# Kernel optimization log

Hardware: AMD Instinct MI355X
Metric: run time of the kernel (lower is better)

The kernel has to match this reference:

```python
import jax, jax.numpy as jnp
import numpy as np

N, E, D_IN, D_E, H, OUT, L = 16384, 131072, 128, 64, 256, 16, 4
EPS_MSG = 1e-7   # GENConv message epsilon
EPS_SM = 1e-16   # PyG softmax denominator epsilon


def _ln(x, g, b, eps=1e-5):
    mu = x.mean(-1, keepdims=True)
    var = x.var(-1, keepdims=True)
    return (x - mu) * jax.lax.rsqrt(var + eps) * g + b


def _genconv(x, src, dst, e, w1, b1, lng, lnb, w2, b2, t):
    # message: relu(x_j + edge_attr) + eps  -> [E, H]
    msg = jax.nn.relu(x[src] + e) + EPS_MSG
    # learnable-temperature segment softmax over incoming edges, per feature
    m = msg * t
    mx = jax.ops.segment_max(m, dst, num_segments=N)
    mx = jnp.where(jnp.isfinite(mx), mx, 0.0)  # empty segments -> 0
    ex = jnp.exp(m - mx[dst])
    den = jax.ops.segment_sum(ex, dst, num_segments=N)
    alpha = ex / (den[dst] + EPS_SM)
    agg = jax.ops.segment_sum(msg * alpha, dst, num_segments=N)  # [N, H]
    # root residual then 2-layer MLP: Linear -> LayerNorm -> ReLU -> Linear
    out = agg + x
    h = jax.nn.relu(_ln(out @ w1 + b1, lng, lnb))
    return h @ w2 + b2


def setup_inputs() -> dict:
    key = jax.random.key(0)
    ks = jax.random.split(key, 10)
    gl = lambda k, shape, fan: jax.random.normal(k, shape, jnp.float32) / np.sqrt(fan).astype(np.float32)
    return {
        "x": jax.random.normal(ks[0], (N, D_IN), jnp.float32),
        "edge_index": jax.random.randint(ks[1], (2, E), 0, N, dtype=jnp.int32),
        "edge_attr": jax.random.normal(ks[2], (E, D_E), jnp.float32),
        "enc_w": gl(ks[3], (D_IN, H), D_IN), "enc_b": jnp.zeros((H,), jnp.float32),
        "ee_w": gl(ks[4], (D_E, H), D_E), "ee_b": jnp.zeros((H,), jnp.float32),
        "w1": gl(ks[5], (L, H, 2 * H), H), "b1": jnp.zeros((L, 2 * H), jnp.float32),
        "lng": jnp.ones((L, 2 * H), jnp.float32), "lnb": jnp.zeros((L, 2 * H), jnp.float32),
        "w2": gl(ks[6], (L, 2 * H, H), 2 * H), "b2": jnp.zeros((L, H), jnp.float32),
        "t": jnp.ones((L,), jnp.float32),
        "ng": jnp.ones((L, H), jnp.float32), "nb": jnp.zeros((L, H), jnp.float32),
        "lin_w": gl(ks[7], (H, OUT), H), "lin_b": jnp.zeros((OUT,), jnp.float32),
    }


def reference(x, edge_index, edge_attr, enc_w, enc_b, ee_w, ee_b,
              w1, b1, lng, lnb, w2, b2, t, ng, nb, lin_w, lin_b):
    src, dst = edge_index[0], edge_index[1]
    h = x @ enc_w + enc_b                      # node encoder
    e = edge_attr @ ee_w + ee_b                # edge encoder
    # first layer: conv only (per source forward)
    h = _genconv(h, src, dst, e, w1[0], b1[0], lng[0], lnb[0], w2[0], b2[0], t[0])
    # remaining layers: res+ block = x + conv(relu(norm(x)))  (dropout off in eval)
    for i in range(1, L):
        z = jax.nn.relu(_ln(h, ng[i], nb[i]))
        h = h + _genconv(z, src, dst, e, w1[i], b1[i], lng[i], lnb[i], w2[i], b2[i], t[i])
    h = jax.nn.relu(_ln(h, ng[0], nb[0]))      # layers[0].act(layers[0].norm(x))
    return h @ lin_w + lin_b
```

## Files before the change

kernel.cpp:

```cpp
#include <hip/hip_runtime.h>
#include <stdint.h>
#include <math.h>


typedef __bf16 bf16x8 __attribute__((ext_vector_type(8)));
typedef __bf16 bf16x4 __attribute__((ext_vector_type(4)));
typedef float  f32x4  __attribute__((ext_vector_type(4)));

constexpr int NN   = 16384;
constexpr int NE   = 131072;
constexpr int DIN  = 128;
constexpr int DE   = 64;
constexpr int HD   = 256;
constexpr int HD2  = 512;

__device__ __forceinline__ void gl_lds16(const __bf16* g, __bf16* l) {
  __builtin_amdgcn_global_load_lds((const __attribute__((address_space(1))) void*)g,
                                   (__attribute__((address_space(3))) void*)l, 16, 0, 0);
}

__global__ __launch_bounds__(1024) void k_scan(const int* __restrict__ deg,
                                               int* __restrict__ row_start) {
  __shared__ int part[1024];
  const int t = threadIdx.x;
  const int base = t * 16;
  int loc[16];
  int s = 0;
  #pragma unroll
  for (int i = 0; i < 16; i++) { loc[i] = s; s += deg[base + i]; }
  part[t] = s;
  __syncthreads();
  for (int off = 1; off < 1024; off <<= 1) {
    int v = (t >= off) ? part[t - off] : 0;
    __syncthreads();
    part[t] += v;
    __syncthreads();
  }
  const int excl = (t == 0) ? 0 : part[t - 1];
  #pragma unroll
  for (int i = 0; i < 16; i++) row_start[base + i] = excl + loc[i];
}

__global__ void k_scatter(const int* __restrict__ src, const int* __restrict__ dst,
                          const int* __restrict__ row_start, int* __restrict__ cursor,
                          int2* __restrict__ csr_es) {
  int e = blockIdx.x * 256 + threadIdx.x;
  if (e >= NE) return;
  const int d = dst[e];
  const int p = atomicAdd(&cursor[d], 1);
  csr_es[row_start[d] + p] = make_int2(e, src[e]);
}

__global__ __launch_bounds__(256)
void k_sortw(const int* __restrict__ row_start, const int* __restrict__ deg,
             int2* __restrict__ csr_es, int* __restrict__ posmap) {
  const int wv   = threadIdx.x >> 6;
  const int lane = threadIdx.x & 63;
  const int node = blockIdx.x * 4 + wv;
  if (node >= NN) return;
  const int st = __builtin_amdgcn_readfirstlane(row_start[node]);
  const int dg = __builtin_amdgcn_readfirstlane(deg[node]);
  if (dg <= 1) {
    if (dg == 1 && lane == 0) posmap[csr_es[st].x] = st;
    return;
  }
  if (dg <= 64) {
    int2 pr = make_int2(0x7fffffff, 0);
    if (lane < dg) pr = csr_es[st + lane];
    int rank = 0;
    for (int j = 0; j < dg; j++) {
      const int ej = __builtin_amdgcn_readlane(pr.x, j);
      if (lane < dg && ej < pr.x) rank++;
    }
    if (lane < dg) {
      csr_es[st + rank] = pr;
      posmap[pr.x] = st + rank;
    }
  } else if (lane == 0) {
    for (int a = 1; a < dg; a++) {
      int2 k = csr_es[st + a];
      int b = a - 1;
      while (b >= 0 && csr_es[st + b].x > k.x) { csr_es[st + b + 1] = csr_es[st + b]; b--; }
      csr_es[st + b + 1] = k;
    }
    for (int a = 0; a < dg; a++) posmap[csr_es[st + a].x] = st + a;
  }
}

__global__ void k_prep(const float* __restrict__ enc_w, const float* __restrict__ ee_w,
                       const float* __restrict__ w1, const float* __restrict__ w2,
                       const int* __restrict__ dst, int* __restrict__ deg,
                       __bf16* __restrict__ enc_wT, __bf16* __restrict__ ee_wT,
                       __bf16* __restrict__ w1T, __bf16* __restrict__ w2T) {
  int i = blockIdx.x * 256 + threadIdx.x;
  const int S0 = DIN * HD, S1 = DE * HD, S2 = 4 * HD * HD2, S3 = 4 * HD2 * HD;
  if (i < S0) { int k = i / HD, n = i % HD; enc_wT[n * DIN + k] = (__bf16)enc_w[i]; return; }
  i -= S0;
  if (i < S1) { int k = i / HD, n = i % HD; ee_wT[n * DE + k] = (__bf16)ee_w[i]; return; }
  i -= S1;
  if (i < S2) {
    int l = i / (HD * HD2), r = i % (HD * HD2), k = r / HD2, n = r % HD2;
    w1T[(size_t)l * HD * HD2 + (size_t)n * HD + k] = (__bf16)w1[i]; return;
  }
  i -= S2;
  if (i < S3) {
    int l = i / (HD2 * HD), r = i % (HD2 * HD), k = r / HD, n = r % HD;
    w2T[(size_t)l * HD2 * HD + (size_t)n * HD2 + k] = (__bf16)w2[i]; return;
  }
  i -= S3;
  if (i < NE) { atomicAdd(&deg[dst[i]], 1); return; }
}

template <int RES, int OBF, int STATS, int ESCAT, int AF32>
__global__ __launch_bounds__(256, 3)
void k_gemm(const void* __restrict__ Ap, const __bf16* __restrict__ BT,
            const float* __restrict__ bias, const float* __restrict__ R,
            float* __restrict__ Cf, __bf16* __restrict__ Cb,
            const int* __restrict__ posmap, float2* __restrict__ pstats,
            int M, int Nn, int K) {
  __shared__ __attribute__((aligned(16))) char smem[32768];
  __bf16* lsA0 = (__bf16*)smem;
  __bf16* lsA1 = (__bf16*)(smem + 8192);
  __bf16* lsB0 = (__bf16*)(smem + 16384);
  __bf16* lsB1 = (__bf16*)(smem + 24576);
  float (*sm)[129] = (float(*)[129])smem;
  float* sbias     = (float*)(smem + 16512);
  float2 (*pst4)[32] = (float2(*)[32])(smem + 17024);
  const __bf16* Ab = (const __bf16*)Ap;
  const float*  Af = (const float*)Ap;
  const int tid  = threadIdx.x;
  const int lane = tid & 63;
  const int wave = tid >> 6;
  const int ntn  = Nn >> 7;
  const int bid  = (int)blockIdx.x;
  const int bn   = (bid >> 3) % ntn;
  const int bm   = (bid & 7) + ((bid >> 3) / ntn) * 8;
  const size_t row0 = (size_t)bm * 128, col0 = (size_t)bn * 128;
  const int wr = (wave >> 1) * 64, wc = (wave & 1) * 64;
  const int ks = lane >> 4, fr = lane & 15;

  f32x4 acc[4][4] = {};

  const int arow = tid >> 2;
  const int aksg = (tid & 3) ^ ((arow >> 1) & 3);

  auto stageB = [&](__bf16* lb, int k0) {
    gl_lds16(BT + (col0 + arow) * K + k0 + aksg * 8, &lb[tid * 8]);
    gl_lds16(BT + (col0 + arow + 64) * K + k0 + aksg * 8, &lb[(tid + 256) * 8]);
  };
  auto stageA = [&](__bf16* la, int k0) {
    gl_lds16(Ab + (row0 + arow) * K + k0 + aksg * 8, &la[tid * 8]);
    gl_lds16(Ab + (row0 + arow + 64) * K + k0 + aksg * 8, &la[(tid + 256) * 8]);
  };
  float4 p0, p1, q0, q1;
  auto loadAf = [&](int k0) {
    const float* a0p = &Af[(row0 + arow) * K + k0 + aksg * 8];
    const float* a1p = &Af[(row0 + arow + 64) * K + k0 + aksg * 8];
    p0 = *(const float4*)a0p; p1 = *(const float4*)(a0p + 4);
    q0 = *(const float4*)a1p; q1 = *(const float4*)(a1p + 4);
  };
  auto writeAf = [&](__bf16* la) {
    bf16x8 o0, o1;
    o0[0] = (__bf16)p0.x; o0[1] = (__bf16)p0.y; o0[2] = (__bf16)p0.z; o0[3] = (__bf16)p0.w;
    o0[4] = (__bf16)p1.x; o0[5] = (__bf16)p1.y; o0[6] = (__bf16)p1.z; o0[7] = (__bf16)p1.w;
    o1[0] = (__bf16)q0.x; o1[1] = (__bf16)q0.y; o1[2] = (__bf16)q0.z; o1[3] = (__bf16)q0.w;
    o1[4] = (__bf16)q1.x; o1[5] = (__bf16)q1.y; o1[6] = (__bf16)q1.z; o1[7] = (__bf16)q1.w;
    *(bf16x8*)&la[tid * 8] = o0;
    *(bf16x8*)&la[(tid + 256) * 8] = o1;
  };

  int slA[4], slB[4];
  #pragma unroll
  for (int m = 0; m < 4; m++) {
    const int rm = wr + m * 16 + fr;
    slA[m] = rm * 4 + (ks ^ ((rm >> 1) & 3));
    const int cn = wc + m * 16 + fr;
    slB[m] = cn * 4 + (ks ^ ((cn >> 1) & 3));
  }

  const int nk = K / 32;
  if (AF32) { loadAf(0); stageB(lsB0, 0); writeAf(lsA0); }
  else      { stageA(lsA0, 0); stageB(lsB0, 0); }
  __syncthreads();
  for (int t = 0; t < nk; t++) {
    const __bf16* la = (t & 1) ? lsA1 : lsA0;
    const __bf16* lb = (t & 1) ? lsB1 : lsB0;
    __bf16* nla = (t & 1) ? lsA0 : lsA1;
    __bf16* nlb = (t & 1) ? lsB0 : lsB1;
    const bool more = (t + 1 < nk);
    if (more) {
      stageB(nlb, (t + 1) * 32);
      if (AF32) loadAf((t + 1) * 32);
      else      stageA(nla, (t + 1) * 32);
    }
    bf16x8 af[4], bfr[4];
    #pragma unroll
    for (int m = 0; m < 4; m++) af[m]  = *(const bf16x8*)&la[slA[m] * 8];
    #pragma unroll
    for (int n = 0; n < 4; n++) bfr[n] = *(const bf16x8*)&lb[slB[n] * 8];
    #pragma unroll
    for (int m = 0; m < 4; m++)
      #pragma unroll
      for (int n = 0; n < 4; n++)
        acc[m][n] = __builtin_amdgcn_mfma_f32_16x16x32_bf16(af[m], bfr[n], acc[m][n], 0, 0, 0);
    if (AF32 && more) writeAf(nla);
    __syncthreads();
  }

  if (tid < 128) sbias[tid] = bias[col0 + tid];
  const int rbase = (wave >> 1) * 16 + ks * 4;
  const int rr = tid >> 3, cs = (tid & 7) * 16;
  #pragma unroll
  for (int m = 0; m < 4; m++) {
    if (m) __syncthreads();
    #pragma unroll
    for (int n = 0; n < 4; n++)
      #pragma unroll
      for (int r = 0; r < 4; r++)
        sm[rbase + r][wc + n * 16 + fr] = acc[m][n][r];
    __syncthreads();
    const size_t lrow = ((rr & 16) ? 64 : 0) + m * 16 + (rr & 15);
    const size_t grow = row0 + lrow;
    float v[16];
    #pragma unroll
    for (int j = 0; j < 16; j++) v[j] = sm[rr][cs + j] + sbias[cs + j];
    if (STATS) {
      float ssum = 0.f, ssq = 0.f;
      #pragma unroll
      for (int j = 0; j < 16; j++) { ssum += v[j]; ssq += v[j] * v[j]; }
      #pragma unroll
      for (int o = 1; o < 8; o <<= 1) {
        ssum += __shfl_xor(ssum, o);
        ssq  += __shfl_xor(ssq, o);
      }
      if ((tid & 7) == 0) pst4[m][rr].x = ssum, pst4[m][rr].y = ssq;
    }
    const size_t gbase = grow * Nn + col0 + cs;
    if (RES) {
      #pragma unroll
      for (int j = 0; j < 16; j += 4) {
        const float4 rv = *(const float4*)&R[gbase + j];
        v[j] += rv.x; v[j + 1] += rv.y; v[j + 2] += rv.z; v[j + 3] += rv.w;
      }
    }
    if (OBF == 0 || OBF == 2) {
      #pragma unroll
      for (int j = 0; j < 16; j += 4) {
        float4 o; o.x = v[j]; o.y = v[j + 1]; o.z = v[j + 2]; o.w = v[j + 3];
        *(float4*)&Cf[gbase + j] = o;
      }
    }
    if (OBF == 1 || OBF == 2) {
      const size_t crow = ESCAT ? (size_t)posmap[grow] : grow;
      const size_t cbase = crow * Nn + col0 + cs;
      bf16x8 o0, o1;
      #pragma unroll
      for (int j = 0; j < 8; j++) { o0[j] = (__bf16)v[j]; o1[j] = (__bf16)v[8 + j]; }
      *(bf16x8*)&Cb[cbase] = o0;
      *(bf16x8*)&Cb[cbase + 8] = o1;
    }
  }
  if (STATS) {
    __syncthreads();
    if (tid < 128) {
      const int lr = tid;
      const int hi = lr >> 6, m2 = (lr >> 4) & 3, rl = lr & 15;
      pstats[(row0 + lr) * ntn + bn] = pst4[m2][(hi << 4) | rl];
    }
  }
}

template <int RES>
__global__ __launch_bounds__(256, 3)
void k_gemm2(const __bf16* __restrict__ c1b, const __bf16* __restrict__ BT,
             const float* __restrict__ bias, const float* __restrict__ R,
             const float2* __restrict__ pstats, const float* __restrict__ gamma,
             const float* __restrict__ beta, float* __restrict__ Cf, int Nn) {
  constexpr int K = HD2;
  __shared__ __attribute__((aligned(16))) char smem[5120 + 32768];
  float* smu  = (float*)smem;
  float* sinv = (float*)(smem + 512);
  float* sg   = (float*)(smem + 1024);
  float* sb   = (float*)(smem + 3072);
  char* arena = smem + 5120;
  __bf16* lsA0 = (__bf16*)arena;
  __bf16* lsA1 = (__bf16*)(arena + 8192);
  __bf16* lsB0 = (__bf16*)(arena + 16384);
  __bf16* lsB1 = (__bf16*)(arena + 24576);
  float (*sm)[129] = (float(*)[129])arena;
  float* sbias     = (float*)(arena + 16512);
  const int tid  = threadIdx.x;
  const int lane = tid & 63;
  const int wave = tid >> 6;
  const int ntn  = Nn >> 7;
  const int bid  = (int)blockIdx.x;
  const int bn   = (bid >> 3) % ntn;
  const int bm   = (bid & 7) + ((bid >> 3) / ntn) * 8;
  const size_t row0 = (size_t)bm * 128, col0 = (size_t)bn * 128;
  const int wr = (wave >> 1) * 64, wc = (wave & 1) * 64;
  const int ks = lane >> 4, fr = lane & 15;

  if (tid < 128) {
    const float4* pp = (const float4*)&pstats[(row0 + tid) * 4];
    const float4 a0 = pp[0], a1 = pp[1];
    const float su = a0.x + a0.z + a1.x + a1.z;
    const float sq = a0.y + a0.w + a1.y + a1.w;
    const float mu = su * (1.f / K);
    const float var = sq * (1.f / K) - mu * mu;
    smu[tid] = mu;
    sinv[tid] = rsqrtf(var + 1e-5f);
  }
  sg[tid] = gamma[tid]; sg[tid + 256] = gamma[tid + 256];
  sb[tid] = beta[tid];  sb[tid + 256] = beta[tid + 256];
  __syncthreads();

  const int arow = tid >> 2;
  const int aksg = (tid & 3) ^ ((arow >> 1) & 3);
  const float muA = smu[arow],      ivA = sinv[arow];
  const float muB = smu[arow + 64], ivB = sinv[arow + 64];
  f32x4 acc[4][4] = {};

  auto stageB = [&](__bf16* lb, int k0) {
    gl_lds16(BT + (col0 + arow) * K + k0 + aksg * 8, &lb[tid * 8]);
    gl_lds16(BT + (col0 + arow + 64) * K + k0 + aksg * 8, &lb[(tid + 256) * 8]);
  };
  auto loadA = [&](int k0, bf16x8& a0, bf16x8& a1v) {
    a0  = *(const bf16x8*)&c1b[(row0 + arow) * K + k0 + aksg * 8];
    a1v = *(const bf16x8*)&c1b[(row0 + arow + 64) * K + k0 + aksg * 8];
  };
  auto writeA = [&](__bf16* la, int k0, const bf16x8& a0, const bf16x8& a1v) {
    const int kb = k0 + aksg * 8;
    bf16x8 o0, o1;
    #pragma unroll
    for (int j = 0; j < 8; j++) {
      const float f0 = ((float)a0[j]  - muA) * ivA * sg[kb + j] + sb[kb + j];
      const float f1 = ((float)a1v[j] - muB) * ivB * sg[kb + j] + sb[kb + j];
      o0[j] = (__bf16)fmaxf(f0, 0.f);
      o1[j] = (__bf16)fmaxf(f1, 0.f);
    }
    *(bf16x8*)&la[tid * 8] = o0;
    *(bf16x8*)&la[(tid + 256) * 8] = o1;
  };

  int slA[4], slB[4];
  #pragma unroll
  for (int m = 0; m < 4; m++) {
    const int rm = wr + m * 16 + fr;
    slA[m] = rm * 4 + (ks ^ ((rm >> 1) & 3));
    const int cn = wc + m * 16 + fr;
    slB[m] = cn * 4 + (ks ^ ((cn >> 1) & 3));
  }

  const int nk = K / 32;
  {
    bf16x8 a0, a1v;
    loadA(0, a0, a1v);
    stageB(lsB0, 0);
    writeA(lsA0, 0, a0, a1v);
  }
  __syncthreads();
  for (int t = 0; t < nk; t++) {
    const __bf16* la = (t & 1) ? lsA1 : lsA0;
    const __bf16* lb = (t & 1) ? lsB1 : lsB0;
    bf16x8 a0, a1v;
    const bool more = (t + 1 < nk);
    if (more) {
      stageB((t & 1) ? lsB0 : lsB1, (t + 1) * 32);
      loadA((t + 1) * 32, a0, a1v);
    }
    bf16x8 af[4], bfr[4];
    #pragma unroll
    for (int m = 0; m < 4; m++) af[m]  = *(const bf16x8*)&la[slA[m] * 8];
    #pragma unroll
    for (int n = 0; n < 4; n++) bfr[n] = *(const bf16x8*)&lb[slB[n] * 8];
    #pragma unroll
    for (int m = 0; m < 4; m++)
      #pragma unroll
      for (int n = 0; n < 4; n++)
        acc[m][n] = __builtin_amdgcn_mfma_f32_16x16x32_bf16(af[m], bfr[n], acc[m][n], 0, 0, 0);
    if (more) writeA((t & 1) ? lsA0 : lsA1, (t + 1) * 32, a0, a1v);
    __syncthreads();
  }

  if (tid < 128) sbias[tid] = bias[col0 + tid];
  const int rbase = (wave >> 1) * 16 + ks * 4;
  const int rr = tid >> 3, cs = (tid & 7) * 16;
  #pragma unroll
  for (int m = 0; m < 4; m++) {
    if (m) __syncthreads();
    #pragma unroll
    for (int n = 0; n < 4; n++)
      #pragma unroll
      for (int r = 0; r < 4; r++)
        sm[rbase + r][wc + n * 16 + fr] = acc[m][n][r];
    __syncthreads();
    const size_t grow = row0 + ((rr & 16) ? 64 : 0) + m * 16 + (rr & 15);
    const size_t gbase = grow * Nn + col0 + cs;
    float v[16];
    #pragma unroll
    for (int j = 0; j < 16; j++) v[j] = sm[rr][cs + j] + sbias[cs + j];
    if (RES) {
      #pragma unroll
      for (int j = 0; j < 16; j += 4) {
        const float4 rv = *(const float4*)&R[gbase + j];
        v[j] += rv.x; v[j + 1] += rv.y; v[j + 2] += rv.z; v[j + 3] += rv.w;
      }
    }
    #pragma unroll
    for (int j = 0; j < 16; j += 4) {
      float4 o; o.x = v[j]; o.y = v[j + 1]; o.z = v[j + 2]; o.w = v[j + 3];
      *(float4*)&Cf[gbase + j] = o;
    }
  }
}

__global__ __launch_bounds__(256)
void k_msg(const __bf16* __restrict__ zb, const __bf16* __restrict__ ecsr,
           const int* __restrict__ row_start, const int* __restrict__ deg,
           const int2* __restrict__ csr_es, const float* __restrict__ tvec,
           int layer, __bf16* __restrict__ a1) {
  const int wv   = __builtin_amdgcn_readfirstlane(threadIdx.x >> 6);
  const int lane = threadIdx.x & 63;
  const int node = blockIdx.x * 4 + wv;
  const int st = __builtin_amdgcn_readfirstlane(row_start[node]);
  const int dg = __builtin_amdgcn_readfirstlane(deg[node]);
  const float t = tvec[layer];
  const int f0 = lane * 4;

  int my_src = 0;
  if (lane < dg) my_src = csr_es[st + lane].y;
  const bf16x4 sv = *(const bf16x4*)&zb[(size_t)node * HD + f0];

  float den[4] = {0.f, 0.f, 0.f, 0.f}, agg[4] = {0.f, 0.f, 0.f, 0.f};
  const int dmain = dg < 64 ? dg : 64;
  int j = 0;
  for (; j + 8 <= dmain; j += 8) {
    bf16x4 zv[8], ev[8];
    #pragma unroll
    for (int u = 0; u < 8; u++) {
      const int sn = __builtin_amdgcn_readlane(my_src, j + u);
      zv[u] = *(const bf16x4*)&zb[(size_t)sn * HD + f0];
      ev[u] = *(const bf16x4*)&ecsr[(size_t)(st + j + u) * HD + f0];
    }
    #pragma unroll
    for (int u = 0; u < 8; u++)
      #pragma unroll
      for (int q = 0; q < 4; q++) {
        const float m  = fmaxf((float)zv[u][q] + (float)ev[u][q], 0.f) + 1e-7f;
        const float ex = __expf(m * t);
        den[q] += ex;
        agg[q] += m * ex;
      }
  }
  for (; j + 4 <= dmain; j += 4) {
    bf16x4 zv[4], ev[4];
    #pragma unroll
    for (int u = 0; u < 4; u++) {
      const int sn = __builtin_amdgcn_readlane(my_src, j + u);
      zv[u] = *(const bf16x4*)&zb[(size_t)sn * HD + f0];
      ev[u] = *(const bf16x4*)&ecsr[(size_t)(st + j + u) * HD + f0];
    }
    #pragma unroll
    for (int u = 0; u < 4; u++)
      #pragma unroll
      for (int q = 0; q < 4; q++) {
        const float m  = fmaxf((float)zv[u][q] + (float)ev[u][q], 0.f) + 1e-7f;
        const float ex = __expf(m * t);
        den[q] += ex;
        agg[q] += m * ex;
      }
  }
  for (; j < dmain; j++) {
    const int sn = __builtin_amdgcn_readlane(my_src, j);
    const bf16x4 zv = *(const bf16x4*)&zb[(size_t)sn * HD + f0];
    const bf16x4 ev = *(const bf16x4*)&ecsr[(size_t)(st + j) * HD + f0];
    #pragma unroll
    for (int q = 0; q < 4; q++) {
      const float m  = fmaxf((float)zv[q] + (float)ev[q], 0.f) + 1e-7f;
      const float ex = __expf(m * t);
      den[q] += ex;
      agg[q] += m * ex;
    }
  }
  for (int jj = 64; jj < dg; jj++) {
    const int2 pr = csr_es[st + jj];
    const bf16x4 zv = *(const bf16x4*)&zb[(size_t)pr.y * HD + f0];
    const bf16x4 ev = *(const bf16x4*)&ecsr[(size_t)(st + jj) * HD + f0];
    #pragma unroll
    for (int q = 0; q < 4; q++) {
      const float m  = fmaxf((float)zv[q] + (float)ev[q], 0.f) + 1e-7f;
      const float ex = __expf(m * t);
      den[q] += ex;
      agg[q] += m * ex;
    }
  }
  bf16x4 r;
  #pragma unroll
  for (int q = 0; q < 4; q++) {
    const float res = (dg > 0) ? agg[q] / (den[q] + 1e-16f) : 0.f;
    r[q] = (__bf16)(res + (float)sv[q]);
  }
  *(bf16x4*)&a1[(size_t)node * HD + f0] = r;
}

__global__ __launch_bounds__(256)
void k_prenorm(const float* __restrict__ h, const float* __restrict__ g,
               const float* __restrict__ b, __bf16* __restrict__ zb) {
  const int row  = blockIdx.x * 4 + (threadIdx.x >> 6);
  const int lane = threadIdx.x & 63;
  const float4 v = *(const float4*)&h[(size_t)row * HD + lane * 4];
  float s = v.x + v.y + v.z + v.w;
  for (int o = 1; o < 64; o <<= 1) s += __shfl_xor(s, o);
  const float mu = s * (1.f / HD);
  const float dx = v.x - mu, dy = v.y - mu, dz = v.z - mu, dw = v.w - mu;
  float q = dx * dx + dy * dy + dz * dz + dw * dw;
  for (int o = 1; o < 64; o <<= 1) q += __shfl_xor(q, o);
  const float inv = rsqrtf(q * (1.f / HD) + 1e-5f);
  const float4 gv = *(const float4*)&g[lane * 4];
  const float4 bv = *(const float4*)&b[lane * 4];
  bf16x4 r;
  r[0] = (__bf16)fmaxf(dx * inv * gv.x + bv.x, 0.f);
  r[1] = (__bf16)fmaxf(dy * inv * gv.y + bv.y, 0.f);
  r[2] = (__bf16)fmaxf(dz * inv * gv.z + bv.z, 0.f);
  r[3] = (__bf16)fmaxf(dw * inv * gv.w + bv.w, 0.f);
  *(bf16x4*)&zb[(size_t)row * HD + lane * 4] = r;
}

__global__ __launch_bounds__(256)
void k_headln(const float* __restrict__ h, const float* __restrict__ g,
              const float* __restrict__ b, const float* __restrict__ lw,
              const float* __restrict__ lb, float* __restrict__ out) {
  __shared__ float slw[256 * 16];
  __shared__ float srow[16 * 256];
  const int t = threadIdx.x;
  const size_t row0 = (size_t)blockIdx.x * 16;
  #pragma unroll
  for (int j = 0; j < 16; j++) slw[j * 256 + t] = lw[j * 256 + t];
  const int rl = t >> 4, col = t & 15;
  float v[16];
  float s = 0.f, sq = 0.f;
  #pragma unroll
  for (int j = 0; j < 16; j += 4) {
    const float4 hv = *(const float4*)&h[(row0 + rl) * HD + col * 16 + j];
    v[j] = hv.x; v[j + 1] = hv.y; v[j + 2] = hv.z; v[j + 3] = hv.w;
  }
  #pragma unroll
  for (int j = 0; j < 16; j++) { s += v[j]; sq += v[j] * v[j]; }
  #pragma unroll
  for (int o = 1; o < 16; o <<= 1) { s += __shfl_xor(s, o); sq += __shfl_xor(sq, o); }
  const float mu = s * (1.f / HD);
  const float inv = rsqrtf(sq * (1.f / HD) - mu * mu + 1e-5f);
  #pragma unroll
  for (int j = 0; j < 16; j += 4) {
    const float4 gv = *(const float4*)&g[col * 16 + j];
    const float4 bv = *(const float4*)&b[col * 16 + j];
    srow[rl * 256 + col * 16 + j]     = fmaxf((v[j]     - mu) * inv * gv.x + bv.x, 0.f);
    srow[rl * 256 + col * 16 + j + 1] = fmaxf((v[j + 1] - mu) * inv * gv.y + bv.y, 0.f);
    srow[rl * 256 + col * 16 + j + 2] = fmaxf((v[j + 2] - mu) * inv * gv.z + bv.z, 0.f);
    srow[rl * 256 + col * 16 + j + 3] = fmaxf((v[j + 3] - mu) * inv * gv.w + bv.w, 0.f);
  }
  __syncthreads();
  float acc = lb[col];
  #pragma unroll 8
  for (int k = 0; k < 256; k++) acc += srow[rl * 256 + k] * slw[k * 16 + col];
  out[(row0 + rl) * 16 + col] = acc;
}

extern "C" void kernel_launch(void* const* d_in, const int* in_sizes, int n_in,
                              void* d_out, int out_size, void* d_ws, size_t ws_size,
                              hipStream_t stream) {
  const float* x     = (const float*)d_in[0];
  const int*   ei    = (const int*)d_in[1];
  const float* ea    = (const float*)d_in[2];
  const float* enc_w = (const float*)d_in[3];
  const float* enc_b = (const float*)d_in[4];
  const float* ee_w  = (const float*)d_in[5];
  const float* ee_b  = (const float*)d_in[6];
  const float* w1    = (const float*)d_in[7];
  const float* b1    = (const float*)d_in[8];
  const float* lng   = (const float*)d_in[9];
  const float* lnb   = (const float*)d_in[10];
  const float* w2    = (const float*)d_in[11];
  const float* b2    = (const float*)d_in[12];
  const float* tvec  = (const float*)d_in[13];
  const float* ng    = (const float*)d_in[14];
  const float* nb    = (const float*)d_in[15];
  const float* lin_w = (const float*)d_in[16];
  const float* lin_b = (const float*)d_in[17];

  uint8_t* p = (uint8_t*)d_ws;
  auto alloc = [&](size_t bytes) { uint8_t* r = p; p += (bytes + 255) & ~(size_t)255; return r; };
  __bf16* e_csr  = (__bf16*)alloc((size_t)NE * HD * 2);
  float*  h      = (float*) alloc((size_t)NN * HD * 4);
  __bf16* hb     = (__bf16*)alloc((size_t)NN * HD * 2);
  __bf16* zb     = (__bf16*)alloc((size_t)NN * HD * 2);
  __bf16* a1     = (__bf16*)alloc((size_t)NN * HD * 2);
  __bf16* c1b    = (__bf16*)alloc((size_t)NN * HD2 * 2);
  float2* pstats = (float2*)alloc((size_t)NN * 4 * 8);
  __bf16* enc_wT = (__bf16*)alloc((size_t)HD * DIN * 2);
  __bf16* ee_wT  = (__bf16*)alloc((size_t)HD * DE * 2);
  __bf16* w1T    = (__bf16*)alloc((size_t)4 * HD2 * HD * 2);
  __bf16* w2T    = (__bf16*)alloc((size_t)4 * HD * HD2 * 2);
  int* deg       = (int*)alloc((size_t)NN * 4);
  int* cursor    = (int*)alloc((size_t)NN * 4);
  int* row_start = (int*)alloc((size_t)NN * 4);
  int* posmap    = (int*)alloc((size_t)NE * 4);
  int2* csr_es   = (int2*)alloc((size_t)NE * 8);

  const int* srcp = ei;
  const int* dstp = ei + NE;

  hipMemsetAsync(deg, 0, (size_t)NN * 8, stream);

  const int prep_total = DIN * HD + DE * HD + 4 * HD * HD2 + 4 * HD2 * HD + NE;
  k_prep<<<(prep_total + 255) / 256, 256, 0, stream>>>(enc_w, ee_w, w1, w2, dstp, deg,
                                                       enc_wT, ee_wT, w1T, w2T);
  k_scan<<<1, 1024, 0, stream>>>(deg, row_start);
  k_scatter<<<NE / 256, 256, 0, stream>>>(srcp, dstp, row_start, cursor, csr_es);
  k_sortw<<<NN / 4, 256, 0, stream>>>(row_start, deg, csr_es, posmap);

  k_gemm<0, 2, 0, 0, 1><<<(NN / 128) * (HD / 128), 256, 0, stream>>>(
      x, enc_wT, enc_b, nullptr, h, hb, nullptr, nullptr, NN, HD, DIN);
  k_gemm<0, 1, 0, 1, 1><<<(NE / 128) * (HD / 128), 256, 0, stream>>>(
      ea, ee_wT, ee_b, nullptr, nullptr, e_csr, posmap, nullptr, NE, HD, DE);

  for (int i = 0; i < 4; i++) {
    const __bf16* zin = (i == 0) ? hb : zb;
    k_msg<<<NN / 4, 256, 0, stream>>>(zin, e_csr, row_start, deg, csr_es, tvec, i, a1);
    k_gemm<0, 1, 1, 0, 0><<<(NN / 128) * (HD2 / 128), 256, 0, stream>>>(
        a1, w1T + (size_t)i * HD2 * HD, b1 + (size_t)i * HD2, nullptr, nullptr, c1b,
        nullptr, pstats, NN, HD2, HD);
    if (i == 0)
      k_gemm2<0><<<(NN / 128) * (HD / 128), 256, 0, stream>>>(
          c1b, w2T + (size_t)i * HD * HD2, b2 + (size_t)i * HD, nullptr, pstats,
          lng + (size_t)i * HD2, lnb + (size_t)i * HD2, h, HD);
    else
      k_gemm2<1><<<(NN / 128) * (HD / 128), 256, 0, stream>>>(
          c1b, w2T + (size_t)i * HD * HD2, b2 + (size_t)i * HD, h, pstats,
          lng + (size_t)i * HD2, lnb + (size_t)i * HD2, h, HD);
    if (i < 3)
      k_prenorm<<<NN / 4, 256, 0, stream>>>(h, ng + (size_t)(i + 1) * HD,
                                            nb + (size_t)(i + 1) * HD, zb);
  }

  k_headln<<<NN / 16, 256, 0, stream>>>(h, ng, nb, lin_w, lin_b, (float*)d_out);
}
```

Before: 337.2 us.

## Triple-buffer LDS in GEMM kernels with explicit vmcnt waits and raw barriers

Both GEMM kernels go from double-buffered to triple-buffered LDS staging. Global loads are issued two K-steps ahead, and partial s_waitcnt vmcnt counts plus raw s_barrier replace __syncthreads, so more loads stay in flight while the MFMAs run. This costs 48KB instead of 32KB of shared memory per block, which may reduce occupancy under launch_bounds(256,3). The hand-tuned waitcnt values must exactly match the number of outstanding loads per thread, so any mismatch risks a race.

```diff
diff --git a/kernel.cpp b/kernel.cpp
--- a/kernel.cpp
+++ b/kernel.cpp
@@ -118,11 +118,7 @@
             float* __restrict__ Cf, __bf16* __restrict__ Cb,
             const int* __restrict__ posmap, float2* __restrict__ pstats,
             int M, int Nn, int K) {
-  __shared__ __attribute__((aligned(16))) char smem[32768];
-  __bf16* lsA0 = (__bf16*)smem;
-  __bf16* lsA1 = (__bf16*)(smem + 8192);
-  __bf16* lsB0 = (__bf16*)(smem + 16384);
-  __bf16* lsB1 = (__bf16*)(smem + 24576);
+  __shared__ __attribute__((aligned(16))) char smem[49152];
   float (*sm)[129] = (float(*)[129])smem;
   float* sbias     = (float*)(smem + 16512);
   float2 (*pst4)[32] = (float2(*)[32])(smem + 17024);
@@ -138,6 +134,9 @@
   const size_t row0 = (size_t)bm * 128, col0 = (size_t)bn * 128;
   const int wr = (wave >> 1) * 64, wc = (wave & 1) * 64;
   const int ks = lane >> 4, fr = lane & 15;
+
+  auto bufA = [&](int i) -> __bf16* { return (__bf16*)(smem + i * 8192); };
+  auto bufB = [&](int i) -> __bf16* { return (__bf16*)(smem + 24576 + i * 8192); };
 
   f32x4 acc[4][4] = {};
 
@@ -179,20 +178,32 @@
   }
 
   const int nk = K / 32;
-  if (AF32) { loadAf(0); stageB(lsB0, 0); writeAf(lsA0); }
-  else      { stageA(lsA0, 0); stageB(lsB0, 0); }
-  __syncthreads();
+  if (AF32) { loadAf(0); stageB(bufB(0), 0); writeAf(bufA(0)); }
+  else      { stageA(bufA(0), 0); stageB(bufB(0), 0); }
+  if (nk > 1) {
+    if (AF32) { loadAf(32); stageB(bufB(1), 32); writeAf(bufA(1)); }
+    else      { stageA(bufA(1), 32); stageB(bufB(1), 32); }
+  }
   for (int t = 0; t < nk; t++) {
-    const __bf16* la = (t & 1) ? lsA1 : lsA0;
-    const __bf16* lb = (t & 1) ? lsB1 : lsB0;
-    __bf16* nla = (t & 1) ? lsA0 : lsA1;
-    __bf16* nlb = (t & 1) ? lsB0 : lsB1;
-    const bool more = (t + 1 < nk);
-    if (more) {
-      stageB(nlb, (t + 1) * 32);
-      if (AF32) loadAf((t + 1) * 32);
-      else      stageA(nla, (t + 1) * 32);
-    }
+    const int rem = nk - 1 - t;
+    const int nb3 = (t + 2) % 3;
+    if (rem >= 2) {
+      if (AF32) { loadAf((t + 2) * 32); stageB(bufB(nb3), (t + 2) * 32); }
+      else      { stageA(bufA(nb3), (t + 2) * 32); stageB(bufB(nb3), (t + 2) * 32); }
+    }
+    if (AF32) {
+      if (rem >= 2)      asm volatile("s_waitcnt vmcnt(8) lgkmcnt(0)" ::: "memory");
+      else if (rem == 1) asm volatile("s_waitcnt vmcnt(2) lgkmcnt(0)" ::: "memory");
+      else               asm volatile("s_waitcnt vmcnt(0) lgkmcnt(0)" ::: "memory");
+    } else {
+      if (rem >= 2)      asm volatile("s_waitcnt vmcnt(8)" ::: "memory");
+      else if (rem == 1) asm volatile("s_waitcnt vmcnt(4)" ::: "memory");
+      else               asm volatile("s_waitcnt vmcnt(0)" ::: "memory");
+    }
+    __builtin_amdgcn_s_barrier();
+    __builtin_amdgcn_sched_barrier(0);
+    const __bf16* la = bufA(t % 3);
+    const __bf16* lb = bufB(t % 3);
     bf16x8 af[4], bfr[4];
     #pragma unroll
     for (int m = 0; m < 4; m++) af[m]  = *(const bf16x8*)&la[slA[m] * 8];
@@ -203,9 +214,10 @@
       #pragma unroll
       for (int n = 0; n < 4; n++)
         acc[m][n] = __builtin_amdgcn_mfma_f32_16x16x32_bf16(af[m], bfr[n], acc[m][n], 0, 0, 0);
-    if (AF32 && more) writeAf(nla);
-    __syncthreads();
-  }
+    if (AF32 && rem >= 2) writeAf(bufA(nb3));
+    __builtin_amdgcn_s_barrier();
+  }
+  __syncthreads();
 
   if (tid < 128) sbias[tid] = bias[col0 + tid];
   const int rbase = (wave >> 1) * 16 + ks * 4;
@@ -277,18 +289,13 @@
              const float2* __restrict__ pstats, const float* __restrict__ gamma,
              const float* __restrict__ beta, float* __restrict__ Cf, int Nn) {
   constexpr int K = HD2;
-  __shared__ __attribute__((aligned(16))) char smem[5120 + 32768];
+  __shared__ __attribute__((aligned(16))) char smem[5120 + 49152];
   float* smu  = (float*)smem;
   float* sinv = (float*)(smem + 512);
   float* sg   = (float*)(smem + 1024);
   float* sb   = (float*)(smem + 3072);
-  char* arena = smem + 5120;
-  __bf16* lsA0 = (__bf16*)arena;
-  __bf16* lsA1 = (__bf16*)(arena + 8192);
-  __bf16* lsB0 = (__bf16*)(arena + 16384);
-  __bf16* lsB1 = (__bf16*)(arena + 24576);
-  float (*sm)[129] = (float(*)[129])arena;
-  float* sbias     = (float*)(arena + 16512);
+  float (*sm)[129] = (float(*)[129])(smem + 5120);
+  float* sbias     = (float*)(smem + 5120 + 16512);
   const int tid  = threadIdx.x;
   const int lane = tid & 63;
   const int wave = tid >> 6;
@@ -299,6 +306,9 @@
   const size_t row0 = (size_t)bm * 128, col0 = (size_t)bn * 128;
   const int wr = (wave >> 1) * 64, wc = (wave & 1) * 64;
   const int ks = lane >> 4, fr = lane & 15;
+
+  auto bufA = [&](int i) -> __bf16* { return (__bf16*)(smem + 5120 + i * 8192); };
+  auto bufB = [&](int i) -> __bf16* { return (__bf16*)(smem + 5120 + 24576 + i * 8192); };
 
   if (tid < 128) {
     const float4* pp = (const float4*)&pstats[(row0 + tid) * 4];
@@ -355,19 +365,27 @@
   {
     bf16x8 a0, a1v;
     loadA(0, a0, a1v);
-    stageB(lsB0, 0);
-    writeA(lsA0, 0, a0, a1v);
-  }
-  __syncthreads();
+    stageB(bufB(0), 0);
+    writeA(bufA(0), 0, a0, a1v);
+    loadA(32, a0, a1v);
+    stageB(bufB(1), 32);
+    writeA(bufA(1), 32, a0, a1v);
+  }
   for (int t = 0; t < nk; t++) {
-    const __bf16* la = (t & 1) ? lsA1 : lsA0;
-    const __bf16* lb = (t & 1) ? lsB1 : lsB0;
+    const int rem = nk - 1 - t;
+    const int nb3 = (t + 2) % 3;
     bf16x8 a0, a1v;
-    const bool more = (t + 1 < nk);
-    if (more) {
-      stageB((t & 1) ? lsB0 : lsB1, (t + 1) * 32);
-      loadA((t + 1) * 32, a0, a1v);
-    }
+    if (rem >= 2) {
+      stageB(bufB(nb3), (t + 2) * 32);
+      loadA((t + 2) * 32, a0, a1v);
+    }
+    if (rem >= 2)      asm volatile("s_waitcnt vmcnt(6) lgkmcnt(0)" ::: "memory");
+    else if (rem == 1) asm volatile("s_waitcnt vmcnt(2) lgkmcnt(0)" ::: "memory");
+    else               asm volatile("s_waitcnt vmcnt(0) lgkmcnt(0)" ::: "memory");
+    __builtin_amdgcn_s_barrier();
+    __builtin_amdgcn_sched_barrier(0);
+    const __bf16* la = bufA(t % 3);
+    const __bf16* lb = bufB(t % 3);
     bf16x8 af[4], bfr[4];
     #pragma unroll
     for (int m = 0; m < 4; m++) af[m]  = *(const bf16x8*)&la[slA[m] * 8];
@@ -378,9 +396,10 @@
       #pragma unroll
       for (int n = 0; n < 4; n++)
         acc[m][n] = __builtin_amdgcn_mfma_f32_16x16x32_bf16(af[m], bfr[n], acc[m][n], 0, 0, 0);
-    if (more) writeA((t & 1) ? lsA0 : lsA1, (t + 1) * 32, a0, a1v);
-    __syncthreads();
-  }
+    if (rem >= 2) writeA(bufA(nb3), (t + 2) * 32, a0, a1v);
+    __builtin_amdgcn_s_barrier();
+  }
+  __syncthreads();
 
   if (tid < 128) sbias[tid] = bias[col0 + tid];
   const int rbase = (wave >> 1) * 16 + ks * 4;
```

Result: no change. 338.6 us (+0.4%).
